# Performance work log

Hardware: AMD Instinct MI355X
Metric: run time of the kernel (lower is better)

## Reference

```python
import jax, jax.numpy as jnp
import numpy as np

N, E, C, EC, L = 50000, 600000, 128, 16, 4
LN_EPS = 1e-5


def setup_inputs() -> dict:
    key = jax.random.key(0)
    ks = jax.random.split(key, 10)
    return {
        "x": jax.random.normal(ks[0], (N, C), jnp.float32),
        "edge_attr": jax.random.normal(ks[1], (E, EC), jnp.float32),
        "We": jax.random.normal(ks[2], (EC, C), jnp.float32) / np.sqrt(EC).astype(np.float32),
        "be": jnp.zeros((C,), jnp.float32),
        "W1": jax.random.normal(ks[3], (L, C, C), jnp.float32) / np.sqrt(C).astype(np.float32),
        "b1": jnp.zeros((L, C), jnp.float32),
        "W2": jax.random.normal(ks[4], (L, C, C), jnp.float32) / np.sqrt(C).astype(np.float32),
        "b2": jnp.zeros((L, C), jnp.float32),
        "gamma": jnp.ones((L, C), jnp.float32),
        "beta": jnp.zeros((L, C), jnp.float32),
        "edge_index": jax.random.randint(ks[5], (2, E), 0, N, dtype=jnp.int32),
    }


def reference(x, edge_attr, We, be, W1, b1, W2, b2, gamma, beta, edge_index):
    src = edge_index[0]  # x_j (message source)
    dst = edge_index[1]  # aggregation target
    # lin_edge: Linear + SiLU, shared across layers
    ea = jax.nn.silu(edge_attr @ We + be)  # [E, C]
    n = x.shape[0]
    for l in range(L):
        # GINEConv message: ReLU(x_j + edge_attr), scatter-sum to target nodes
        msg = jax.nn.relu(x[src] + ea)                       # [E, C]
        agg = jax.ops.segment_sum(msg, dst, num_segments=n)  # [N, C]
        h = x + agg  # (1 + eps) * x + agg, eps = 0
        # GINEConv nn: Linear -> SiLU -> Linear
        h = jax.nn.silu(h @ W1[l] + b1[l]) @ W2[l] + b2[l]
        # residual + LayerNorm
        y = x + h
        mu = y.mean(-1, keepdims=True)
        var = y.var(-1, keepdims=True)
        x = (y - mu) * jax.lax.rsqrt(var + LN_EPS) * gamma[l] + beta[l]
    return x
```

## Files before the change

### kernel.cpp

```cpp
#include <hip/hip_runtime.h>

#define NN 50000
#define EE 600000
#define CC 128
#define ECC 16
#define LL 4
#define LN_EPS 1e-5f
#define MTILE 80
#define PADC 136
#define YSTR 132

typedef float f32x4 __attribute__((ext_vector_type(4)));
typedef short bf16x8 __attribute__((ext_vector_type(8)));

static __device__ __forceinline__ float bf2f(unsigned short u) {
  union { unsigned int i; float f; } v; v.i = ((unsigned int)u) << 16; return v.f;
}
static __device__ __forceinline__ unsigned short f2bf(float f) {
  union { float f; unsigned int i; } v; v.f = f;
  unsigned int b = v.i + 0x7FFFu + ((v.i >> 16) & 1u);
  return (unsigned short)(b >> 16);
}
static __device__ __forceinline__ float silu_f(float v) {
  return v / (1.f + __expf(-v));
}


__global__ void count_kernel(const int* __restrict__ dst, int* __restrict__ counts, int E) {
  int e = blockIdx.x * blockDim.x + threadIdx.x;
  if (e < E) atomicAdd(&counts[dst[e]], 1);
}

__global__ __launch_bounds__(1024) void scan1_kernel(const int* __restrict__ counts,
                                                     int* __restrict__ bsum, int n) {
  __shared__ int wsum[16];
  const int tid = threadIdx.x, lane = tid & 63, wv = tid >> 6;
  const int i = blockIdx.x * 1024 + tid;
  int s = (i < n) ? counts[i] : 0;
  #pragma unroll
  for (int off = 1; off < 64; off <<= 1) s += __shfl_xor(s, off);
  if (lane == 0) wsum[wv] = s;
  __syncthreads();
  if (tid == 0) {
    int t = 0;
    #pragma unroll
    for (int j = 0; j < 16; ++j) t += wsum[j];
    bsum[blockIdx.x] = t;
  }
}

__global__ void scan2_kernel(const int* __restrict__ bsum, int* __restrict__ boff, int nb) {
  const int lane = threadIdx.x;
  int v = (lane < nb) ? bsum[lane] : 0;
  int incl = v;
  #pragma unroll
  for (int off = 1; off < 64; off <<= 1) {
    int t = __shfl_up(incl, off);
    if (lane >= off) incl += t;
  }
  if (lane < nb) boff[lane] = incl - v;
}

__global__ __launch_bounds__(1024) void scan3_kernel(const int* __restrict__ counts,
                                                     const int* __restrict__ boff,
                                                     int* __restrict__ rowptr, int n) {
  __shared__ int wsum[16];
  const int tid = threadIdx.x, lane = tid & 63, wv = tid >> 6;
  const int i = blockIdx.x * 1024 + tid;
  const int v = (i < n) ? counts[i] : 0;
  int incl = v;
  #pragma unroll
  for (int off = 1; off < 64; off <<= 1) {
    int t = __shfl_up(incl, off);
    if (lane >= off) incl += t;
  }
  if (lane == 63) wsum[wv] = incl;
  __syncthreads();
  if (wv == 0) {
    int vv = (lane < 16) ? wsum[lane] : 0;
    int vi = vv;
    #pragma unroll
    for (int off = 1; off < 16; off <<= 1) {
      int t = __shfl_up(vi, off);
      if (lane >= off) vi += t;
    }
    if (lane < 16) wsum[lane] = vi - vv;
  }
  __syncthreads();
  if (i < n) rowptr[i + 1] = boff[blockIdx.x] + wsum[wv] + incl;
  if (i == 0) rowptr[0] = 0;
}

__global__ void fill_kernel(const int* __restrict__ src, const int* __restrict__ dst,
                            const int* __restrict__ rowptr, int* __restrict__ cursor,
                            int* __restrict__ eidx, int* __restrict__ esrc, int E) {
  int e = blockIdx.x * blockDim.x + threadIdx.x;
  if (e < E) {
    const int d = dst[e];
    const int pos = rowptr[d] + atomicAdd(&cursor[d], 1);
    eidx[pos] = e;
    esrc[pos] = src[e];
  }
}


__global__ void webconv_kernel(const float* __restrict__ We, unsigned short* __restrict__ webf) {
  const int t = blockIdx.x * blockDim.x + threadIdx.x;
  if (t >= 8 * 64 * 8) return;
  const int j = t & 7, l = (t >> 3) & 63, cg = t >> 9;
  const int k = (l >> 4) * 8 + j, c = cg * 16 + (l & 15);
  webf[t] = (k < 16) ? f2bf(We[k * CC + c]) : (unsigned short)0;
}


__global__ __launch_bounds__(256) void ea_kernel(const float* __restrict__ edge_attr,
                                                 const unsigned short* __restrict__ webf,
                                                 const float* __restrict__ be,
                                                 const int* __restrict__ eidx,
                                                 unsigned short* __restrict__ ea) {
  __shared__ float er[64][20];
  __shared__ unsigned short eaT[64 * 132];
  const int tid = threadIdx.x;
  const int lane = tid & 63, wv = tid >> 6;

  bf16x8 bw[8];
  #pragma unroll
  for (int cg = 0; cg < 8; ++cg)
    bw[cg] = *(const bf16x8*)(webf + cg * 512 + lane * 8);
  float bev[8];
  #pragma unroll
  for (int cg = 0; cg < 8; ++cg) bev[cg] = be[cg * 16 + (lane & 15)];

  const int base = blockIdx.x * 64;
  {
    const int r = tid >> 2, q = tid & 3;
    const int e = eidx[base + r];
    *(float4*)(&er[r][q * 4]) = *(const float4*)(edge_attr + (size_t)e * ECC + q * 4);
  }
  __syncthreads();

  const int arow = wv * 16 + (lane & 15);
  const int ko = lane >> 4;
  union { unsigned short u[8]; bf16x8 v; } afu;
  if (ko < 2) {
    #pragma unroll
    for (int j = 0; j < 8; ++j) afu.u[j] = f2bf(er[arow][ko * 8 + j]);
  } else {
    #pragma unroll
    for (int j = 0; j < 8; ++j) afu.u[j] = 0;
  }

  f32x4 acc[8];
  #pragma unroll
  for (int cg = 0; cg < 8; ++cg) {
    acc[cg] = (f32x4)0.f;
    acc[cg] = __builtin_amdgcn_mfma_f32_16x16x32_bf16(afu.v, bw[cg], acc[cg], 0, 0, 0);
  }

  const int rl0 = wv * 16 + ko * 4;
  const int cb = lane & 15;
  #pragma unroll
  for (int cg = 0; cg < 8; ++cg)
    #pragma unroll
    for (int r = 0; r < 4; ++r) {
      const float v = acc[cg][r] + bev[cg];
      eaT[(rl0 + r) * 132 + cg * 16 + cb] = f2bf(silu_f(v));
    }
  __syncthreads();

  uint4* eg = (uint4*)(ea + (size_t)base * CC);
  #pragma unroll
  for (int k = 0; k < 4; ++k) {
    const int u = tid + k * 256;
    const int row = u >> 4, ch = u & 15;
    eg[u] = *(const uint4*)(&eaT[row * 132 + ch * 8]);
  }
}


__global__ __launch_bounds__(128) void wconv_kernel(const float* __restrict__ W1,
                                                    const float* __restrict__ W2,
                                                    unsigned short* __restrict__ wt) {
  const int b = blockIdx.x;
  const int c = b & (CC - 1);
  const int mat = (b >> 7) & 1;
  const int l = b >> 8;
  const float* W = (mat ? W2 : W1) + (size_t)l * CC * CC;
  unsigned short* o = wt + ((size_t)l * 2 + mat) * CC * CC + (size_t)c * CC;
  const int k = threadIdx.x;
  o[k] = f2bf(W[(size_t)k * CC + c]);
}


__global__ __launch_bounds__(256) void agg2_kernel(const float* __restrict__ x_in,
                                                   unsigned short* __restrict__ h_out,
                                                   const unsigned int* __restrict__ ea32,
                                                   const int* __restrict__ rowptr,
                                                   const int* __restrict__ esrc) {
  const int tid = threadIdx.x;
  const int lane = tid & 63;
  const int wv = tid >> 6;
  const int n = blockIdx.x * 4 + wv;

  const int p0 = rowptr[n], p1 = rowptr[n + 1];
  float ax = 0.f, ay = 0.f;
  int p = p0;
  for (; p + 4 <= p1; p += 4) {
    const int s0 = esrc[p], s1 = esrc[p + 1], s2 = esrc[p + 2], s3 = esrc[p + 3];
    const float2 x0 = *(const float2*)(x_in + (size_t)s0 * CC + lane * 2);
    const float2 x1 = *(const float2*)(x_in + (size_t)s1 * CC + lane * 2);
    const float2 x2 = *(const float2*)(x_in + (size_t)s2 * CC + lane * 2);
    const float2 x3 = *(const float2*)(x_in + (size_t)s3 * CC + lane * 2);
    const unsigned int e0 = ea32[(size_t)p * 64 + lane];
    const unsigned int e1 = ea32[(size_t)(p + 1) * 64 + lane];
    const unsigned int e2 = ea32[(size_t)(p + 2) * 64 + lane];
    const unsigned int e3 = ea32[(size_t)(p + 3) * 64 + lane];
    ax += fmaxf(x0.x + bf2f((unsigned short)e0), 0.f)
        + fmaxf(x1.x + bf2f((unsigned short)e1), 0.f)
        + fmaxf(x2.x + bf2f((unsigned short)e2), 0.f)
        + fmaxf(x3.x + bf2f((unsigned short)e3), 0.f);
    ay += fmaxf(x0.y + bf2f((unsigned short)(e0 >> 16)), 0.f)
        + fmaxf(x1.y + bf2f((unsigned short)(e1 >> 16)), 0.f)
        + fmaxf(x2.y + bf2f((unsigned short)(e2 >> 16)), 0.f)
        + fmaxf(x3.y + bf2f((unsigned short)(e3 >> 16)), 0.f);
  }
  for (; p < p1; ++p) {
    const int s0 = esrc[p];
    const float2 x0 = *(const float2*)(x_in + (size_t)s0 * CC + lane * 2);
    const unsigned int e0 = ea32[(size_t)p * 64 + lane];
    ax += fmaxf(x0.x + bf2f((unsigned short)e0), 0.f);
    ay += fmaxf(x0.y + bf2f((unsigned short)(e0 >> 16)), 0.f);
  }
  const float2 xs = *(const float2*)(x_in + (size_t)n * CC + lane * 2);
  const unsigned int packed =
      (unsigned int)f2bf(xs.x + ax) | ((unsigned int)f2bf(xs.y + ay) << 16);
  *(unsigned int*)(h_out + (size_t)n * CC + lane * 2) = packed;
}


__global__ __launch_bounds__(256) void agg_fb_kernel(const float* __restrict__ x_in,
                                                     unsigned short* __restrict__ h_out,
                                                     const float* __restrict__ edge_attr,
                                                     const float* __restrict__ We,
                                                     const float* __restrict__ be,
                                                     const int* __restrict__ rowptr,
                                                     const int* __restrict__ eidx,
                                                     const int* __restrict__ esrc) {
  const int tid = threadIdx.x;
  const int c = tid & (CC - 1);
  const int g = tid >> 7;
  const int n = blockIdx.x * 2 + g;

  float wec[ECC];
  #pragma unroll
  for (int k = 0; k < ECC; ++k) wec[k] = We[k * CC + c];
  const float bev = be[c];

  const int p0 = rowptr[n], p1 = rowptr[n + 1];
  float acc = 0.f;
  for (int p = p0; p < p1; ++p) {
    const int e0 = eidx[p];
    const int s0 = esrc[p];
    const float4* ar0 = (const float4*)(edge_attr + (size_t)e0 * ECC);
    const float4 a0 = ar0[0], a1 = ar0[1], a2 = ar0[2], a3 = ar0[3];
    float v0 = bev
      + a0.x*wec[0]  + a0.y*wec[1]  + a0.z*wec[2]  + a0.w*wec[3]
      + a1.x*wec[4]  + a1.y*wec[5]  + a1.z*wec[6]  + a1.w*wec[7]
      + a2.x*wec[8]  + a2.y*wec[9]  + a2.z*wec[10] + a2.w*wec[11]
      + a3.x*wec[12] + a3.y*wec[13] + a3.z*wec[14] + a3.w*wec[15];
    acc += fmaxf(x_in[(size_t)s0 * CC + c] + silu_f(v0), 0.f);
  }
  h_out[(size_t)n * CC + c] = f2bf(x_in[(size_t)n * CC + c] + acc);
}


__global__ __launch_bounds__(256) void mlp_kernel(const float* __restrict__ x_in,
                                                  const unsigned short* __restrict__ hbuf,
                                                  const unsigned short* __restrict__ wt1,
                                                  const unsigned short* __restrict__ wt2,
                                                  const float* __restrict__ b1,
                                                  const float* __restrict__ b2,
                                                  const float* __restrict__ gamma,
                                                  const float* __restrict__ beta,
                                                  float* __restrict__ x_out) {
  __shared__ __align__(16) char smem[MTILE * PADC * 2 * 2];
  unsigned short* hA = (unsigned short*)smem;
  unsigned short* tA = (unsigned short*)(smem + MTILE * PADC * 2);
  float* yS = (float*)smem;
  __shared__ float red[MTILE][4][2];

  const int tid = threadIdx.x;
  const int lane = tid & 63;
  const int wv = tid >> 6;
  const int node0 = blockIdx.x * MTILE;
  const int colq = lane & 15;
  const int krow = lane >> 4;
  const int colb = wv * 32;

  for (int idx = tid; idx < MTILE * 16; idx += 256) {
    const int row = idx >> 4, ch = idx & 15;
    *(uint4*)(&hA[row * PADC + ch * 8]) =
        *(const uint4*)(hbuf + (size_t)(node0 + row) * CC + ch * 8);
  }
  __syncthreads();

  bf16x8 bw[2][4];
  #pragma unroll
  for (int n2 = 0; n2 < 2; ++n2)
    #pragma unroll
    for (int kk = 0; kk < 4; ++kk)
      bw[n2][kk] = *(const bf16x8*)(wt1 + (size_t)(colb + n2 * 16 + colq) * CC + kk * 32 + krow * 8);

  f32x4 acc[5][2];
  #pragma unroll
  for (int m = 0; m < 5; ++m) { acc[m][0] = (f32x4)0.f; acc[m][1] = (f32x4)0.f; }

  #pragma unroll
  for (int m = 0; m < 5; ++m)
    #pragma unroll
    for (int kk = 0; kk < 4; ++kk) {
      const bf16x8 a = *(const bf16x8*)(&hA[(m * 16 + colq) * PADC + kk * 32 + krow * 8]);
      acc[m][0] = __builtin_amdgcn_mfma_f32_16x16x32_bf16(a, bw[0][kk], acc[m][0], 0, 0, 0);
      acc[m][1] = __builtin_amdgcn_mfma_f32_16x16x32_bf16(a, bw[1][kk], acc[m][1], 0, 0, 0);
    }

  const float b1v0 = b1[colb + colq], b1v1 = b1[colb + 16 + colq];
  #pragma unroll
  for (int m = 0; m < 5; ++m)
    #pragma unroll
    for (int r = 0; r < 4; ++r) {
      const int row = m * 16 + krow * 4 + r;
      tA[row * PADC + colb + colq]      = f2bf(silu_f(acc[m][0][r] + b1v0));
      tA[row * PADC + colb + 16 + colq] = f2bf(silu_f(acc[m][1][r] + b1v1));
    }
  __syncthreads();

  #pragma unroll
  for (int n2 = 0; n2 < 2; ++n2)
    #pragma unroll
    for (int kk = 0; kk < 4; ++kk)
      bw[n2][kk] = *(const bf16x8*)(wt2 + (size_t)(colb + n2 * 16 + colq) * CC + kk * 32 + krow * 8);

  f32x4 acc2[5][2];
  #pragma unroll
  for (int m = 0; m < 5; ++m) { acc2[m][0] = (f32x4)0.f; acc2[m][1] = (f32x4)0.f; }

  #pragma unroll
  for (int m = 0; m < 5; ++m)
    #pragma unroll
    for (int kk = 0; kk < 4; ++kk) {
      const bf16x8 a = *(const bf16x8*)(&tA[(m * 16 + colq) * PADC + kk * 32 + krow * 8]);
      acc2[m][0] = __builtin_amdgcn_mfma_f32_16x16x32_bf16(a, bw[0][kk], acc2[m][0], 0, 0, 0);
      acc2[m][1] = __builtin_amdgcn_mfma_f32_16x16x32_bf16(a, bw[1][kk], acc2[m][1], 0, 0, 0);
    }

  const float b2v0 = b2[colb + colq], b2v1 = b2[colb + 16 + colq];
  float yv[5][2][4];
  #pragma unroll
  for (int m = 0; m < 5; ++m)
    #pragma unroll
    for (int r = 0; r < 4; ++r) {
      const int row = m * 16 + krow * 4 + r;
      yv[m][0][r] = acc2[m][0][r] + b2v0 + x_in[(size_t)(node0 + row) * CC + colb + colq];
      yv[m][1][r] = acc2[m][1][r] + b2v1 + x_in[(size_t)(node0 + row) * CC + colb + 16 + colq];
    }

  #pragma unroll
  for (int m = 0; m < 5; ++m)
    #pragma unroll
    for (int r = 0; r < 4; ++r) {
      float s = yv[m][0][r] + yv[m][1][r];
      float s2 = yv[m][0][r] * yv[m][0][r] + yv[m][1][r] * yv[m][1][r];
      #pragma unroll
      for (int off = 1; off < 16; off <<= 1) {
        s  += __shfl_xor(s, off);
        s2 += __shfl_xor(s2, off);
      }
      if (colq == 0) {
        const int row = m * 16 + krow * 4 + r;
        red[row][wv][0] = s;
        red[row][wv][1] = s2;
      }
    }
  __syncthreads();

  const float gm0 = gamma[colb + colq], gm1 = gamma[colb + 16 + colq];
  const float bt0 = beta[colb + colq],  bt1 = beta[colb + 16 + colq];
  #pragma unroll
  for (int m = 0; m < 5; ++m)
    #pragma unroll
    for (int r = 0; r < 4; ++r) {
      const int row = m * 16 + krow * 4 + r;
      const float s  = red[row][0][0] + red[row][1][0] + red[row][2][0] + red[row][3][0];
      const float s2 = red[row][0][1] + red[row][1][1] + red[row][2][1] + red[row][3][1];
      const float mean = s * (1.f / 128.f);
      const float var = s2 * (1.f / 128.f) - mean * mean;
      const float rstd = rsqrtf(var + LN_EPS);
      yS[row * YSTR + colb + colq]      = (yv[m][0][r] - mean) * rstd * gm0 + bt0;
      yS[row * YSTR + colb + 16 + colq] = (yv[m][1][r] - mean) * rstd * gm1 + bt1;
    }
  __syncthreads();

  float* og = x_out + (size_t)node0 * CC;
  #pragma unroll
  for (int k = 0; k < 10; ++k) {
    const int u = tid + k * 256;
    const int row = u >> 5, q = u & 31;
    *(float4*)(og + u * 4) = *(const float4*)(&yS[row * YSTR + q * 4]);
  }
}


extern "C" void kernel_launch(void* const* d_in, const int* in_sizes, int n_in,
                              void* d_out, int out_size, void* d_ws, size_t ws_size,
                              hipStream_t stream) {
  const float* x         = (const float*)d_in[0];
  const float* edge_attr = (const float*)d_in[1];
  const float* We        = (const float*)d_in[2];
  const float* be        = (const float*)d_in[3];
  const float* W1        = (const float*)d_in[4];
  const float* b1        = (const float*)d_in[5];
  const float* W2        = (const float*)d_in[6];
  const float* b2        = (const float*)d_in[7];
  const float* gamma     = (const float*)d_in[8];
  const float* beta      = (const float*)d_in[9];
  const int*   ei        = (const int*)d_in[10];
  const int*   src       = ei;
  const int*   dst       = ei + EE;
  float* out = (float*)d_out;

  char* ws = (char*)d_ws;
  float*          xbuf   = (float*)(ws + 0);
  unsigned short* hbuf   = (unsigned short*)(ws + 25600000);
  unsigned short* wt     = (unsigned short*)(ws + 38400000);
  int*            counts = (int*)(ws + 38662400);
  int*            rowptr = (int*)(ws + 38862592);
  int*            cursor = (int*)(ws + 39062784);
  int*            eidx   = (int*)(ws + 39262976);
  int*            esrc   = (int*)(ws + 41663232);
  unsigned short* ea     = (unsigned short*)(ws + 44063232);
  unsigned short* webf   = (unsigned short*)(ws + 39062784);
  int*            bsum   = (int*)(ws + 39262976);
  int*            boff   = (int*)(ws + 39262976 + 256);
  const bool use_ea = (ws_size >= 197663232ull);
  const int NB = (NN + 1023) / 1024;

  hipMemsetAsync(counts, 0, (size_t)NN * 4, stream);
  hipMemsetAsync(cursor, 0, (size_t)NN * 4, stream);
  count_kernel<<<(EE + 255) / 256, 256, 0, stream>>>(dst, counts, EE);
  scan1_kernel<<<NB, 1024, 0, stream>>>(counts, bsum, NN);
  scan2_kernel<<<1, 64, 0, stream>>>(bsum, boff, NB);
  scan3_kernel<<<NB, 1024, 0, stream>>>(counts, boff, rowptr, NN);
  fill_kernel<<<(EE + 255) / 256, 256, 0, stream>>>(src, dst, rowptr, cursor, eidx, esrc, EE);
  wconv_kernel<<<LL * 2 * CC, 128, 0, stream>>>(W1, W2, wt);
  if (use_ea) {
    webconv_kernel<<<16, 256, 0, stream>>>(We, webf);
    ea_kernel<<<EE / 64, 256, 0, stream>>>(edge_attr, webf, be, eidx, ea);
  }

  const float* xin = x;
  float* bufs[LL] = { xbuf, out, xbuf, out };
  for (int l = 0; l < LL; ++l) {
    float* xo = bufs[l];
    if (use_ea)
      agg2_kernel<<<NN / 4, 256, 0, stream>>>(xin, hbuf, (const unsigned int*)ea, rowptr, esrc);
    else
      agg_fb_kernel<<<NN / 2, 256, 0, stream>>>(xin, hbuf, edge_attr, We, be, rowptr, eidx, esrc);
    mlp_kernel<<<NN / MTILE, 256, 0, stream>>>(
        xin, hbuf,
        wt + ((size_t)l * 2) * CC * CC, wt + ((size_t)l * 2 + 1) * CC * CC,
        b1 + (size_t)l * CC, b2 + (size_t)l * CC,
        gamma + (size_t)l * CC, beta + (size_t)l * CC, xo);
    xin = xo;
  }
}
```

Baseline: 489.5 us.

## Recompute edge embeddings inside aggregation instead of materializing bf16 edge features

```diff
diff --git a/kernel.cpp b/kernel.cpp
--- a/kernel.cpp
+++ b/kernel.cpp
@@ -9,6 +9,7 @@
 #define MTILE 80
 #define PADC 136
 #define YSTR 132
+#define AGG_BLOCKS 2048
 
 typedef float f32x4 __attribute__((ext_vector_type(4)));
 typedef short bf16x8 __attribute__((ext_vector_type(8)));
@@ -23,6 +24,22 @@
 }
 static __device__ __forceinline__ float silu_f(float v) {
   return v / (1.f + __expf(-v));
+}
+
+static __device__ __forceinline__ float2 dot16_2(const float4 a0, const float4 a1,
+                                                 const float4 a2, const float4 a3,
+                                                 const float2* __restrict__ w,
+                                                 const float2 b) {
+  float vx = b.x, vy = b.y;
+  vx += a0.x*w[0].x  + a0.y*w[1].x  + a0.z*w[2].x  + a0.w*w[3].x
+      + a1.x*w[4].x  + a1.y*w[5].x  + a1.z*w[6].x  + a1.w*w[7].x
+      + a2.x*w[8].x  + a2.y*w[9].x  + a2.z*w[10].x + a2.w*w[11].x
+      + a3.x*w[12].x + a3.y*w[13].x + a3.z*w[14].x + a3.w*w[15].x;
+  vy += a0.x*w[0].y  + a0.y*w[1].y  + a0.z*w[2].y  + a0.w*w[3].y
+      + a1.x*w[4].y  + a1.y*w[5].y  + a1.z*w[6].y  + a1.w*w[7].y
+      + a2.x*w[8].y  + a2.y*w[9].y  + a2.z*w[10].y + a2.w*w[11].y
+      + a3.x*w[12].y + a3.y*w[13].y + a3.z*w[14].y + a3.w*w[15].y;
+  return make_float2(vx, vy);
 }
 
 
@@ -104,77 +121,15 @@
 }
 
 
-__global__ void webconv_kernel(const float* __restrict__ We, unsigned short* __restrict__ webf) {
-  const int t = blockIdx.x * blockDim.x + threadIdx.x;
-  if (t >= 8 * 64 * 8) return;
-  const int j = t & 7, l = (t >> 3) & 63, cg = t >> 9;
-  const int k = (l >> 4) * 8 + j, c = cg * 16 + (l & 15);
-  webf[t] = (k < 16) ? f2bf(We[k * CC + c]) : (unsigned short)0;
-}
-
-
-__global__ __launch_bounds__(256) void ea_kernel(const float* __restrict__ edge_attr,
-                                                 const unsigned short* __restrict__ webf,
-                                                 const float* __restrict__ be,
-                                                 const int* __restrict__ eidx,
-                                                 unsigned short* __restrict__ ea) {
-  __shared__ float er[64][20];
-  __shared__ unsigned short eaT[64 * 132];
-  const int tid = threadIdx.x;
-  const int lane = tid & 63, wv = tid >> 6;
-
-  bf16x8 bw[8];
-  #pragma unroll
-  for (int cg = 0; cg < 8; ++cg)
-    bw[cg] = *(const bf16x8*)(webf + cg * 512 + lane * 8);
-  float bev[8];
-  #pragma unroll
-  for (int cg = 0; cg < 8; ++cg) bev[cg] = be[cg * 16 + (lane & 15)];
-
-  const int base = blockIdx.x * 64;
-  {
-    const int r = tid >> 2, q = tid & 3;
-    const int e = eidx[base + r];
-    *(float4*)(&er[r][q * 4]) = *(const float4*)(edge_attr + (size_t)e * ECC + q * 4);
-  }
-  __syncthreads();
-
-  const int arow = wv * 16 + (lane & 15);
-  const int ko = lane >> 4;
-  union { unsigned short u[8]; bf16x8 v; } afu;
-  if (ko < 2) {
-    #pragma unroll
-    for (int j = 0; j < 8; ++j) afu.u[j] = f2bf(er[arow][ko * 8 + j]);
-  } else {
-    #pragma unroll
-    for (int j = 0; j < 8; ++j) afu.u[j] = 0;
-  }
-
-  f32x4 acc[8];
-  #pragma unroll
-  for (int cg = 0; cg < 8; ++cg) {
-    acc[cg] = (f32x4)0.f;
-    acc[cg] = __builtin_amdgcn_mfma_f32_16x16x32_bf16(afu.v, bw[cg], acc[cg], 0, 0, 0);
-  }
-
-  const int rl0 = wv * 16 + ko * 4;
-  const int cb = lane & 15;
-  #pragma unroll
-  for (int cg = 0; cg < 8; ++cg)
-    #pragma unroll
-    for (int r = 0; r < 4; ++r) {
-      const float v = acc[cg][r] + bev[cg];
-      eaT[(rl0 + r) * 132 + cg * 16 + cb] = f2bf(silu_f(v));
-    }
-  __syncthreads();
-
-  uint4* eg = (uint4*)(ea + (size_t)base * CC);
-  #pragma unroll
-  for (int k = 0; k < 4; ++k) {
-    const int u = tid + k * 256;
-    const int row = u >> 4, ch = u & 15;
-    eg[u] = *(const uint4*)(&eaT[row * 132 + ch * 8]);
-  }
+__global__ __launch_bounds__(256) void gather_attr_kernel(const float* __restrict__ edge_attr,
+                                                          const int* __restrict__ eidx,
+                                                          float* __restrict__ attr_csr) {
+  const long t = (long)blockIdx.x * 256 + threadIdx.x;
+  if (t >= (long)EE * 4) return;
+  const int p = (int)(t >> 2), q = (int)(t & 3);
+  const int e = eidx[p];
+  *(float4*)(attr_csr + (size_t)p * ECC + q * 4) =
+      *(const float4*)(edge_attr + (size_t)e * ECC + q * 4);
 }
 
 
@@ -192,49 +147,54 @@
 }
 
 
-__global__ __launch_bounds__(256) void agg2_kernel(const float* __restrict__ x_in,
+__global__ __launch_bounds__(256) void agg3_kernel(const float* __restrict__ x_in,
                                                    unsigned short* __restrict__ h_out,
-                                                   const unsigned int* __restrict__ ea32,
+                                                   const float* __restrict__ attr_csr,
+                                                   const float* __restrict__ We,
+                                                   const float* __restrict__ be,
                                                    const int* __restrict__ rowptr,
                                                    const int* __restrict__ esrc) {
   const int tid = threadIdx.x;
   const int lane = tid & 63;
   const int wv = tid >> 6;
-  const int n = blockIdx.x * 4 + wv;
-
-  const int p0 = rowptr[n], p1 = rowptr[n + 1];
-  float ax = 0.f, ay = 0.f;
-  int p = p0;
-  for (; p + 4 <= p1; p += 4) {
-    const int s0 = esrc[p], s1 = esrc[p + 1], s2 = esrc[p + 2], s3 = esrc[p + 3];
-    const float2 x0 = *(const float2*)(x_in + (size_t)s0 * CC + lane * 2);
-    const float2 x1 = *(const float2*)(x_in + (size_t)s1 * CC + lane * 2);
-    const float2 x2 = *(const float2*)(x_in + (size_t)s2 * CC + lane * 2);
-    const float2 x3 = *(const float2*)(x_in + (size_t)s3 * CC + lane * 2);
-    const unsigned int e0 = ea32[(size_t)p * 64 + lane];
-    const unsigned int e1 = ea32[(size_t)(p + 1) * 64 + lane];
-    const unsigned int e2 = ea32[(size_t)(p + 2) * 64 + lane];
-    const unsigned int e3 = ea32[(size_t)(p + 3) * 64 + lane];
-    ax += fmaxf(x0.x + bf2f((unsigned short)e0), 0.f)
-        + fmaxf(x1.x + bf2f((unsigned short)e1), 0.f)
-        + fmaxf(x2.x + bf2f((unsigned short)e2), 0.f)
-        + fmaxf(x3.x + bf2f((unsigned short)e3), 0.f);
-    ay += fmaxf(x0.y + bf2f((unsigned short)(e0 >> 16)), 0.f)
-        + fmaxf(x1.y + bf2f((unsigned short)(e1 >> 16)), 0.f)
-        + fmaxf(x2.y + bf2f((unsigned short)(e2 >> 16)), 0.f)
-        + fmaxf(x3.y + bf2f((unsigned short)(e3 >> 16)), 0.f);
-  }
-  for (; p < p1; ++p) {
-    const int s0 = esrc[p];
-    const float2 x0 = *(const float2*)(x_in + (size_t)s0 * CC + lane * 2);
-    const unsigned int e0 = ea32[(size_t)p * 64 + lane];
-    ax += fmaxf(x0.x + bf2f((unsigned short)e0), 0.f);
-    ay += fmaxf(x0.y + bf2f((unsigned short)(e0 >> 16)), 0.f);
-  }
-  const float2 xs = *(const float2*)(x_in + (size_t)n * CC + lane * 2);
-  const unsigned int packed =
-      (unsigned int)f2bf(xs.x + ax) | ((unsigned int)f2bf(xs.y + ay) << 16);
-  *(unsigned int*)(h_out + (size_t)n * CC + lane * 2) = packed;
+  const int c0 = lane * 2;
+
+  float2 wec[ECC];
+  #pragma unroll
+  for (int k = 0; k < ECC; ++k) wec[k] = *(const float2*)(We + k * CC + c0);
+  const float2 bev = *(const float2*)(be + c0);
+
+  const int wid = blockIdx.x * 4 + wv;
+  const int nw = AGG_BLOCKS * 4;
+  for (int n = wid; n < NN; n += nw) {
+    const int p0 = rowptr[n], p1 = rowptr[n + 1];
+    float ax = 0.f, ay = 0.f;
+    int p = p0;
+    for (; p + 2 <= p1; p += 2) {
+      const int s0 = esrc[p], s1 = esrc[p + 1];
+      const float2 x0 = *(const float2*)(x_in + (size_t)s0 * CC + c0);
+      const float2 x1 = *(const float2*)(x_in + (size_t)s1 * CC + c0);
+      const float4* ar = (const float4*)(attr_csr + (size_t)p * ECC);
+      const float4 a0 = ar[0], a1 = ar[1], a2 = ar[2], a3 = ar[3];
+      const float4 b0 = ar[4], b1 = ar[5], b2 = ar[6], b3 = ar[7];
+      const float2 v0 = dot16_2(a0, a1, a2, a3, wec, bev);
+      const float2 v1 = dot16_2(b0, b1, b2, b3, wec, bev);
+      ax += fmaxf(x0.x + silu_f(v0.x), 0.f) + fmaxf(x1.x + silu_f(v1.x), 0.f);
+      ay += fmaxf(x0.y + silu_f(v0.y), 0.f) + fmaxf(x1.y + silu_f(v1.y), 0.f);
+    }
+    if (p < p1) {
+      const int s0 = esrc[p];
+      const float2 x0 = *(const float2*)(x_in + (size_t)s0 * CC + c0);
+      const float4* ar = (const float4*)(attr_csr + (size_t)p * ECC);
+      const float2 v0 = dot16_2(ar[0], ar[1], ar[2], ar[3], wec, bev);
+      ax += fmaxf(x0.x + silu_f(v0.x), 0.f);
+      ay += fmaxf(x0.y + silu_f(v0.y), 0.f);
+    }
+    const float2 xs = *(const float2*)(x_in + (size_t)n * CC + c0);
+    const unsigned int packed =
+        (unsigned int)f2bf(xs.x + ax) | ((unsigned int)f2bf(xs.y + ay) << 16);
+    *(unsigned int*)(h_out + (size_t)n * CC + c0) = packed;
+  }
 }
 
 
@@ -438,11 +398,10 @@
   int*            cursor = (int*)(ws + 39062784);
   int*            eidx   = (int*)(ws + 39262976);
   int*            esrc   = (int*)(ws + 41663232);
-  unsigned short* ea     = (unsigned short*)(ws + 44063232);
-  unsigned short* webf   = (unsigned short*)(ws + 39062784);
+  float*          attr_csr = (float*)(ws + 44063232);
   int*            bsum   = (int*)(ws + 39262976);
   int*            boff   = (int*)(ws + 39262976 + 256);
-  const bool use_ea = (ws_size >= 197663232ull);
+  const bool use_fast = (ws_size >= 82463232ull);
   const int NB = (NN + 1023) / 1024;
 
   hipMemsetAsync(counts, 0, (size_t)NN * 4, stream);
@@ -453,17 +412,15 @@
   scan3_kernel<<<NB, 1024, 0, stream>>>(counts, boff, rowptr, NN);
   fill_kernel<<<(EE + 255) / 256, 256, 0, stream>>>(src, dst, rowptr, cursor, eidx, esrc, EE);
   wconv_kernel<<<LL * 2 * CC, 128, 0, stream>>>(W1, W2, wt);
-  if (use_ea) {
-    webconv_kernel<<<16, 256, 0, stream>>>(We, webf);
-    ea_kernel<<<EE / 64, 256, 0, stream>>>(edge_attr, webf, be, eidx, ea);
-  }
+  if (use_fast)
+    gather_attr_kernel<<<(EE * 4 + 255) / 256, 256, 0, stream>>>(edge_attr, eidx, attr_csr);
 
   const float* xin = x;
   float* bufs[LL] = { xbuf, out, xbuf, out };
   for (int l = 0; l < LL; ++l) {
     float* xo = bufs[l];
-    if (use_ea)
-      agg2_kernel<<<NN / 4, 256, 0, stream>>>(xin, hbuf, (const unsigned int*)ea, rowptr, esrc);
+    if (use_fast)
+      agg3_kernel<<<AGG_BLOCKS, 256, 0, stream>>>(xin, hbuf, attr_csr, We, be, rowptr, esrc);
     else
       agg_fb_kernel<<<NN / 2, 256, 0, stream>>>(xin, hbuf, edge_attr, We, be, rowptr, eidx, esrc);
     mlp_kernel<<<NN / MTILE, 256, 0, stream>>>(
```

Result: slower. 682.6 us (+39.4%).
